# Kernel optimization log

Measured on AMD Instinct MI355X. Metric: run time of the kernel, lower is better.

The kernel has to match this reference:

```python
import jax, jax.numpy as jnp
import numpy as np

SUBSTEP = 10
FRAMES = 24
T = FRAMES * SUBSTEP
DT = 1.0 / 60.0 / SUBSTEP
SLOPE_DEG = 20.0
COS_S = float(np.cos(np.deg2rad(SLOPE_DEG)))
SIN_S = float(np.sin(np.deg2rad(SLOPE_DEG)))
INIT_HEIGHT = 0.1
N_VERTS = 2_000_000
GRAVITY = jnp.array([0.0, -9.8, 0.0], dtype=jnp.float32)
CONTACT_N = jnp.array([-SIN_S, COS_S, 0.0], dtype=jnp.float32)
EPS = 1e-6


def quat_mul(a, b):
    w1, x1, y1, z1 = a[0], a[1], a[2], a[3]
    w2, x2, y2, z2 = b[0], b[1], b[2], b[3]
    return jnp.stack([
        w1 * w2 - x1 * x2 - y1 * y2 - z1 * z2,
        w1 * x2 + x1 * w2 + y1 * z2 - z1 * y2,
        w1 * y2 + y1 * w2 + z1 * x2 - x1 * z2,
        w1 * z2 + z1 * w2 + x1 * y2 - y1 * x2,
    ])


def quat_to_matrix(q):
    q = q / jnp.linalg.norm(q)
    w, x, y, z = q[0], q[1], q[2], q[3]
    return jnp.stack([
        jnp.stack([1 - 2 * y * y - 2 * z * z, 2 * x * y - 2 * w * z, 2 * x * z + 2 * w * y]),
        jnp.stack([2 * x * y + 2 * w * z, 1 - 2 * x * x - 2 * z * z, 2 * y * z - 2 * w * x]),
        jnp.stack([2 * x * z - 2 * w * y, 2 * y * z + 2 * w * x, 1 - 2 * x * x - 2 * y * y]),
    ])


def cross_matrix(a):
    z = jnp.zeros((), dtype=a.dtype)
    return jnp.stack([
        jnp.stack([z, -a[2], a[1]]),
        jnp.stack([a[2], z, -a[0]]),
        jnp.stack([-a[1], a[0], z]),
    ])


def setup_inputs() -> dict:
    key = jax.random.key(0)
    k1, k2, k3 = jax.random.split(key, 3)
    return {
        "x": jax.random.normal(k1, (N_VERTS, 3), dtype=jnp.float32) * 0.2,
        "mass_center": jnp.zeros((3,), dtype=jnp.float32),
        "init_trans": jax.random.normal(k2, (3,), dtype=jnp.float32) * 0.3 + jnp.array([0.3, 0.5, 0.0]),
        "init_quat": jnp.ones((4,), dtype=jnp.float32),
        "init_v": jax.random.normal(k3, (3,), dtype=jnp.float32) * 0.1,
        "kn": jnp.array([0.5], dtype=jnp.float32),
        "mu": jnp.array([0.4], dtype=jnp.float32),
        "linear_damping": jnp.array([0.999], dtype=jnp.float32),
        "angular_damping": jnp.array([0.998], dtype=jnp.float32),
    }


def _simulate(x, mass_center, init_trans, init_quat, init_v, kn, mu, linear_damping, angular_damping):
    n = x.shape[0]
    mass = jnp.asarray(float(n), dtype=x.dtype)  # unit mass per vertex
    inv_mass = 1.0 / mass
    r = x - mass_center
    # inertia_reference = sum_i m*( (r.r) I - outer(r,r) )
    inertia = jnp.sum(jnp.einsum('ni,ni->n', r, r)) * jnp.eye(3, dtype=x.dtype) - jnp.einsum('ni,nj->ij', r, r)
    kn0, mu0 = kn[0], mu[0]
    ld, ad = linear_damping[0], angular_damping[0]
    eye3 = jnp.eye(3, dtype=x.dtype)

    def step(carry, _):
        trans, quat, v, omega = carry
        Rm = quat_to_matrix(quat)
        Rx = x @ Rm.T                                   # [N,3]
        xi = trans + Rx + mass_center                   # world positions
        vi_all = v + jnp.cross(omega[None, :], Rx)      # per-vertex velocities
        d = xi @ CONTACT_N
        rel_v = vi_all @ CONTACT_N
        mask = (d < -COS_S * INIT_HEIGHT) & (rel_v < 0.0)
        num = jnp.sum(mask)
        numf = jnp.maximum(num, 1).astype(x.dtype)
        sum_pos = jnp.sum(x * mask[:, None].astype(x.dtype), axis=0)
        ri = sum_pos / numf
        Ri = Rm @ ri
        vi = v + jnp.cross(omega, Ri)
        v_n = jnp.dot(vi, CONTACT_N) * CONTACT_N
        v_t = vi - v_n
        vn_new = -kn0 * v_n
        alpha = jnp.maximum(1.0 - mu0 * (1.0 + kn0) * (jnp.linalg.norm(v_n) / (jnp.linalg.norm(v_t) + EPS)), 0.0)
        vi_new = vn_new + alpha * v_t
        I = Rm @ inertia @ Rm.T
        I_inv = jnp.linalg.inv(I)
        Rri = cross_matrix(Ri)
        kmat = inv_mass * eye3 - Rri @ I_inv @ Rri
        J = jnp.linalg.solve(kmat, vi_new - vi)
        hit = num > 0
        dv = jnp.where(hit, J * inv_mass, 0.0)
        domega = jnp.where(hit, I_inv @ Rri @ J, 0.0)
        v_new = (v + GRAVITY * DT) * ld + dv
        omega_new = omega * ad + domega
        trans_new = trans + DT * v_new
        wq = jnp.concatenate([jnp.zeros((1,), dtype=x.dtype), omega_new]) * (0.5 * DT)
        quat_new = quat + quat_mul(wq, quat)
        quat_new = quat_new / jnp.linalg.norm(quat_new)
        new_carry = (trans_new, quat_new, v_new, omega_new)
        return new_carry, jnp.concatenate([trans_new, quat_new])

    carry0 = (init_trans, init_quat / jnp.linalg.norm(init_quat), init_v, jnp.zeros(3, dtype=x.dtype))
    _, traj = jax.lax.scan(step, carry0, None, length=T)
    return traj  # [T, 7] = translation(3) + quaternion(4) per substep


def reference(x, mass_center, init_trans, init_quat, init_v, kn, mu, linear_damping, angular_damping):
    return _simulate(x, mass_center, init_trans, init_quat, init_v, kn, mu, linear_damping, angular_damping)
```

## Files before the change

### kernel.cpp

```cpp
#include <hip/hip_runtime.h>

#define GRID   256
#define BLOCK  512
#define NWAVES (BLOCK / 64)
#define CHUNK  7813
#define SLOTS  16
#define NREPT  64

typedef unsigned long long u64;

__device__ __forceinline__ u64 rec_load(const u64* p) {
  return __hip_atomic_load(p, __ATOMIC_RELAXED, __HIP_MEMORY_SCOPE_AGENT);
}
__device__ __forceinline__ void rec_store(u64* p, u64 v) {
  __hip_atomic_store(p, v, __ATOMIC_RELAXED, __HIP_MEMORY_SCOPE_AGENT);
}
__device__ __forceinline__ u64 rec_pack(float f, unsigned tag) {
  return (u64)__float_as_uint(f) | ((u64)tag << 32);
}

#define C_NX   ((float)(-0.3420201433256687))
#define C_NY   ((float)( 0.9396926207859084))
#define C_DTF  ((float)(1.0 / 60.0 / 10.0))
#define C_HDT  ((float)(0.5 * (1.0 / 60.0 / 10.0)))
#define C_DTH  ((float)(-0.9396926207859084 * 0.1))
#define C_GYDT (-9.8f * (float)(1.0 / 60.0 / 10.0))

__device__ __forceinline__ void mat3_mul(const float* A, const float* B, float* C) {
  #pragma unroll
  for (int i = 0; i < 3; ++i)
    #pragma unroll
    for (int j = 0; j < 3; ++j)
      C[i*3+j] = A[i*3+0]*B[0*3+j] + A[i*3+1]*B[1*3+j] + A[i*3+2]*B[2*3+j];
}
__device__ __forceinline__ void mat3_mul_bt(const float* A, const float* B, float* C) {
  #pragma unroll
  for (int i = 0; i < 3; ++i)
    #pragma unroll
    for (int j = 0; j < 3; ++j)
      C[i*3+j] = A[i*3+0]*B[j*3+0] + A[i*3+1]*B[j*3+1] + A[i*3+2]*B[j*3+2];
}
__device__ __forceinline__ void mat3_inv(const float* m, float* inv) {
  float A =  (m[4]*m[8] - m[5]*m[7]);
  float B = -(m[3]*m[8] - m[5]*m[6]);
  float C =  (m[3]*m[7] - m[4]*m[6]);
  float det = m[0]*A + m[1]*B + m[2]*C;
  float id = 1.0f / det;
  inv[0] = A * id;
  inv[1] = -(m[1]*m[8] - m[2]*m[7]) * id;
  inv[2] =  (m[1]*m[5] - m[2]*m[4]) * id;
  inv[3] = B * id;
  inv[4] =  (m[0]*m[8] - m[2]*m[6]) * id;
  inv[5] = -(m[0]*m[5] - m[2]*m[3]) * id;
  inv[6] = C * id;
  inv[7] = -(m[0]*m[7] - m[1]*m[6]) * id;
  inv[8] =  (m[0]*m[4] - m[1]*m[3]) * id;
}

__global__ __launch_bounds__(BLOCK, 2)
void sim_kernel(const float* __restrict__ xg,
                const float* __restrict__ mc_p,
                const float* __restrict__ itr_p,
                const float* __restrict__ iq_p,
                const float* __restrict__ iv_p,
                const float* __restrict__ kn_p,
                const float* __restrict__ mu_p,
                const float* __restrict__ ldp_p,
                const float* __restrict__ adp_p,
                float* __restrict__ out,
                u64* __restrict__ ws,
                int N, int T)
{
  const int tid  = threadIdx.x;
  const int bid  = blockIdx.x;
  const int lane = tid & 63;
  const int wid  = tid >> 6;

  __shared__ float s_redI[NWAVES * 6];
  __shared__ float s_red[2][NWAVES * 4];
  __shared__ float s_gat[NWAVES * 4];

  u64* part = ws;
  u64* tot  = ws + 2 * 4 * GRID;
  u64* bufI = ws + 2 * 4 * GRID + 2 * NREPT * 4;

  const float mc0 = mc_p[0], mc1 = mc_p[1], mc2 = mc_p[2];

  const int vstart = bid * CHUNK;
  int cl = N - vstart; if (cl > CHUNK) cl = CHUNK; if (cl < 0) cl = 0;

  const float NANF = __int_as_float(0x7fc00000);
  float xr0[SLOTS], xr1[SLOTS], xr2[SLOTS];
  #pragma unroll
  for (int s = 0; s < SLOTS; ++s) {
    const int i = tid + s * BLOCK;
    if (i < cl) {
      const float* p = xg + (size_t)(vstart + i) * 3;
      xr0[s] = p[0]; xr1[s] = p[1]; xr2[s] = p[2];
    } else {
      xr0[s] = NANF; xr1[s] = NANF; xr2[s] = NANF;
    }
  }

  {
    float v6[6] = {0,0,0,0,0,0};
    #pragma unroll
    for (int s = 0; s < SLOTS; ++s) {
      if (tid + s * BLOCK < cl) {
        float r0 = xr0[s] - mc0, r1 = xr1[s] - mc1, r2 = xr2[s] - mc2;
        v6[0] += r0*r0; v6[1] += r1*r1; v6[2] += r2*r2;
        v6[3] += r0*r1; v6[4] += r0*r2; v6[5] += r1*r2;
      }
    }
    #pragma unroll
    for (int off = 32; off > 0; off >>= 1)
      #pragma unroll
      for (int k = 0; k < 6; ++k) v6[k] += __shfl_down(v6[k], off, 64);
    if (lane == 0) {
      #pragma unroll
      for (int k = 0; k < 6; ++k) s_redI[wid * 6 + k] = v6[k];
    }
    __syncthreads();
    if (tid == 0) {
      float t6[6];
      #pragma unroll
      for (int k = 0; k < 6; ++k) {
        t6[k] = s_redI[k];
        #pragma unroll
        for (int w = 1; w < NWAVES; ++w) t6[k] += s_redI[w * 6 + k];
      }
      #pragma unroll
      for (int k = 0; k < 6; ++k) rec_store(bufI + k * GRID + bid, rec_pack(t6[k], 0xC0FFEEu));
    }
    __syncthreads();
  }

  float In[9];
  {
    float g6[6] = {0,0,0,0,0,0};
    if (tid < GRID) {
      u64 r[6];
      int f = 0;
      for (;;) {
        #pragma unroll
        for (int k = 0; k < 6; ++k) r[k] = rec_load(bufI + k * GRID + tid);
        bool ok = true;
        #pragma unroll
        for (int k = 0; k < 6; ++k) ok &= ((unsigned)(r[k] >> 32) == 0xC0FFEEu);
        if (ok) break;
        if ((++f & 15) == 0) __builtin_amdgcn_s_sleep(1);
      }
      #pragma unroll
      for (int k = 0; k < 6; ++k) g6[k] = __uint_as_float((unsigned)r[k]);
    }
    #pragma unroll
    for (int off = 32; off > 0; off >>= 1)
      #pragma unroll
      for (int k = 0; k < 6; ++k) g6[k] += __shfl_down(g6[k], off, 64);
    if (lane == 0) {
      #pragma unroll
      for (int k = 0; k < 6; ++k) s_redI[wid * 6 + k] = g6[k];
    }
    __syncthreads();
    float t6[6];
    #pragma unroll
    for (int k = 0; k < 6; ++k) {
      t6[k] = s_redI[k];
      #pragma unroll
      for (int w = 1; w < NWAVES; ++w) t6[k] += s_redI[w * 6 + k];
    }
    float trc = t6[0] + t6[1] + t6[2];
    In[0] = trc - t6[0]; In[4] = trc - t6[1]; In[8] = trc - t6[2];
    In[1] = -t6[3]; In[3] = -t6[3];
    In[2] = -t6[4]; In[6] = -t6[4];
    In[5] = -t6[5]; In[7] = -t6[5];
  }

  float tr0 = itr_p[0], tr1 = itr_p[1], tr2 = itr_p[2];
  float q0 = iq_p[0], q1 = iq_p[1], q2 = iq_p[2], q3 = iq_p[3];
  {
    float n0 = sqrtf(q0*q0 + q1*q1 + q2*q2 + q3*q3);
    q0 /= n0; q1 /= n0; q2 /= n0; q3 /= n0;
  }
  float v0 = iv_p[0], v1 = iv_p[1], v2 = iv_p[2];
  float om0 = 0.f, om1 = 0.f, om2 = 0.f;
  const float knv = kn_p[0], muv = mu_p[0], ldv = ldp_p[0], adv = adp_p[0];
  const float inv_mass = 1.0f / (float)N;

  float Rm[9], Ii[9];
  float pa0, pa1, pa2, pb0, pb1, pb2, pca, pcb;
  int skip;

  {
    float qn = sqrtf(q0*q0 + q1*q1 + q2*q2 + q3*q3);
    float w = q0/qn, xq = q1/qn, yq = q2/qn, zq = q3/qn;
    Rm[0] = 1.f - 2.f*yq*yq - 2.f*zq*zq; Rm[1] = 2.f*xq*yq - 2.f*w*zq; Rm[2] = 2.f*xq*zq + 2.f*w*yq;
    Rm[3] = 2.f*xq*yq + 2.f*w*zq; Rm[4] = 1.f - 2.f*xq*xq - 2.f*zq*zq; Rm[5] = 2.f*yq*zq - 2.f*w*xq;
    Rm[6] = 2.f*xq*zq - 2.f*w*yq; Rm[7] = 2.f*yq*zq + 2.f*w*xq; Rm[8] = 1.f - 2.f*xq*xq - 2.f*yq*yq;
    pa0 = Rm[0]*C_NX + Rm[3]*C_NY;
    pa1 = Rm[1]*C_NX + Rm[4]*C_NY;
    pa2 = Rm[2]*C_NX + Rm[5]*C_NY;
    float w0 = C_NY*om2, w1 = -C_NX*om2, w2 = C_NX*om1 - C_NY*om0;
    pb0 = Rm[0]*w0 + Rm[3]*w1 + Rm[6]*w2;
    pb1 = Rm[1]*w0 + Rm[4]*w1 + Rm[7]*w2;
    pb2 = Rm[2]*w0 + Rm[5]*w1 + Rm[8]*w2;
    pca = C_DTH - ((tr0 + mc0)*C_NX + (tr1 + mc1)*C_NY);
    pcb = -(v0*C_NX + v1*C_NY);
    skip = (om0 == 0.f && om1 == 0.f && om2 == 0.f && !(pcb > 0.f)) ? 1 : 0;
    float Tm[9]; mat3_mul(Rm, In, Tm);
    float Iw[9]; mat3_mul_bt(Tm, Rm, Iw);
    mat3_inv(Iw, Ii);
  }

  int pub = 0;
  for (int t = 0; t < T; ++t) {
    float tn = 0.f, tx = 0.f, ty = 0.f, tz = 0.f;

    if (!skip) {
      const int p = pub & 1;
      const unsigned want = (unsigned)(pub + 1);

      float acc0 = 0.f, acc1 = 0.f, acc2 = 0.f, acc3 = 0.f;
      #pragma unroll
      for (int s = 0; s < SLOTS; ++s) {
        const float x0 = xr0[s], x1 = xr1[s], x2 = xr2[s];
        const float da = x0*pa0 + x1*pa1 + x2*pa2;
        const float db = x0*pb0 + x1*pb1 + x2*pb2;
        if (da < pca && db < pcb) {
          acc0 += 1.f; acc1 += x0; acc2 += x1; acc3 += x2;
        }
      }
      #pragma unroll
      for (int off = 32; off > 0; off >>= 1) {
        acc0 += __shfl_down(acc0, off, 64);
        acc1 += __shfl_down(acc1, off, 64);
        acc2 += __shfl_down(acc2, off, 64);
        acc3 += __shfl_down(acc3, off, 64);
      }
      float* srA = s_red[p];
      if (lane == 0) {
        srA[wid*4+0] = acc0; srA[wid*4+1] = acc1;
        srA[wid*4+2] = acc2; srA[wid*4+3] = acc3;
      }
      __syncthreads();
      if (tid < 4) {
        float tw = srA[tid];
        #pragma unroll
        for (int w2 = 1; w2 < NWAVES; ++w2) tw += srA[w2*4 + tid];
        rec_store(part + (size_t)p * 4 * GRID + (size_t)tid * GRID + bid,
                  rec_pack(tw, want));
      }

      {
        float Tm[9]; mat3_mul(Rm, In, Tm);
        float Iw[9]; mat3_mul_bt(Tm, Rm, Iw);
        mat3_inv(Iw, Ii);
      }

      if (bid == 0) {
        float f0 = 0.f, f1 = 0.f, f2 = 0.f, f3 = 0.f;
        if (tid < GRID) {
          const u64* pp = part + (size_t)p * 4 * GRID + tid;
          u64 r0, r1, r2, r3;
          int fl = 0;
          for (;;) {
            r0 = rec_load(pp + 0 * GRID);
            r1 = rec_load(pp + 1 * GRID);
            r2 = rec_load(pp + 2 * GRID);
            r3 = rec_load(pp + 3 * GRID);
            if (((unsigned)(r0 >> 32) == want) && ((unsigned)(r1 >> 32) == want) &&
                ((unsigned)(r2 >> 32) == want) && ((unsigned)(r3 >> 32) == want)) break;
            if ((++fl & 15) == 0) __builtin_amdgcn_s_sleep(1);
          }
          f0 = __uint_as_float((unsigned)r0);
          f1 = __uint_as_float((unsigned)r1);
          f2 = __uint_as_float((unsigned)r2);
          f3 = __uint_as_float((unsigned)r3);
        }
        #pragma unroll
        for (int off = 32; off > 0; off >>= 1) {
          f0 += __shfl_down(f0, off, 64);
          f1 += __shfl_down(f1, off, 64);
          f2 += __shfl_down(f2, off, 64);
          f3 += __shfl_down(f3, off, 64);
        }
        if (lane == 0) {
          s_gat[wid*4+0] = f0; s_gat[wid*4+1] = f1;
          s_gat[wid*4+2] = f2; s_gat[wid*4+3] = f3;
        }
        __syncthreads();
        tn = s_gat[0]; tx = s_gat[1]; ty = s_gat[2]; tz = s_gat[3];
        #pragma unroll
        for (int w2 = 1; w2 < NWAVES; ++w2) {
          tn += s_gat[w2*4+0]; tx += s_gat[w2*4+1];
          ty += s_gat[w2*4+2]; tz += s_gat[w2*4+3];
        }
        if (tid < NREPT * 4) {
          const int w2 = tid & 3;
          const float val = (w2 == 0) ? tn : (w2 == 1) ? tx : (w2 == 2) ? ty : tz;
          rec_store(tot + (size_t)p * NREPT * 4 + tid, rec_pack(val, want));
        }
      } else {
        const u64* tp = tot + (size_t)p * NREPT * 4 + (size_t)(bid & (NREPT - 1)) * 4;
        u64 r0, r1, r2, r3;
        int fl = 0;
        for (;;) {
          r0 = rec_load(tp + 0); r1 = rec_load(tp + 1);
          r2 = rec_load(tp + 2); r3 = rec_load(tp + 3);
          if (((unsigned)(r0 >> 32) == want) && ((unsigned)(r1 >> 32) == want) &&
              ((unsigned)(r2 >> 32) == want) && ((unsigned)(r3 >> 32) == want)) break;
          if ((++fl & 31) == 0) __builtin_amdgcn_s_sleep(1);
        }
        tn = __uint_as_float((unsigned)r0);
        tx = __uint_as_float((unsigned)r1);
        ty = __uint_as_float((unsigned)r2);
        tz = __uint_as_float((unsigned)r3);
      }
      ++pub;
    }

    {
      float dv0 = 0.f, dv1 = 0.f, dv2 = 0.f, dm0 = 0.f, dm1 = 0.f, dm2 = 0.f;
      if (tn > 0.0f) {
        float numf = fmaxf(tn, 1.0f);
        float ri0 = tx/numf, ri1 = ty/numf, ri2 = tz/numf;
        float Ri0 = Rm[0]*ri0 + Rm[1]*ri1 + Rm[2]*ri2;
        float Ri1 = Rm[3]*ri0 + Rm[4]*ri1 + Rm[5]*ri2;
        float Ri2 = Rm[6]*ri0 + Rm[7]*ri1 + Rm[8]*ri2;
        float vi0 = v0 + om1*Ri2 - om2*Ri1;
        float vi1 = v1 + om2*Ri0 - om0*Ri2;
        float vi2 = v2 + om0*Ri1 - om1*Ri0;
        float vdn = vi0*C_NX + vi1*C_NY;
        float vn0 = vdn*C_NX, vn1 = vdn*C_NY;
        float vt0 = vi0 - vn0, vt1 = vi1 - vn1, vt2 = vi2;
        float nvn = sqrtf(vn0*vn0 + vn1*vn1);
        float nvt = sqrtf(vt0*vt0 + vt1*vt1 + vt2*vt2);
        float alpha = fmaxf(1.0f - muv*(1.0f + knv)*(nvn/(nvt + 1e-6f)), 0.0f);
        float dvi0 = (-knv*vn0 + alpha*vt0) - vi0;
        float dvi1 = (-knv*vn1 + alpha*vt1) - vi1;
        float dvi2 = (alpha*vt2) - vi2;
        float Cx[9] = {0.f, -Ri2, Ri1,  Ri2, 0.f, -Ri0,  -Ri1, Ri0, 0.f};
        float T2[9]; mat3_mul(Cx, Ii, T2);
        float T3[9]; mat3_mul(T2, Cx, T3);
        float Km[9];
        #pragma unroll
        for (int m = 0; m < 9; ++m) Km[m] = -T3[m];
        Km[0] += inv_mass; Km[4] += inv_mass; Km[8] += inv_mass;
        float Ki[9]; mat3_inv(Km, Ki);
        float J0 = Ki[0]*dvi0 + Ki[1]*dvi1 + Ki[2]*dvi2;
        float J1 = Ki[3]*dvi0 + Ki[4]*dvi1 + Ki[5]*dvi2;
        float J2 = Ki[6]*dvi0 + Ki[7]*dvi1 + Ki[8]*dvi2;
        dv0 = J0*inv_mass; dv1 = J1*inv_mass; dv2 = J2*inv_mass;
        float c0 = -Ri2*J1 + Ri1*J2;
        float c1 =  Ri2*J0 - Ri0*J2;
        float c2 = -Ri1*J0 + Ri0*J1;
        dm0 = Ii[0]*c0 + Ii[1]*c1 + Ii[2]*c2;
        dm1 = Ii[3]*c0 + Ii[4]*c1 + Ii[5]*c2;
        dm2 = Ii[6]*c0 + Ii[7]*c1 + Ii[8]*c2;
      }
      v0 = v0*ldv + dv0;
      v1 = (v1 + C_GYDT)*ldv + dv1;
      v2 = v2*ldv + dv2;
      om0 = om0*adv + dm0; om1 = om1*adv + dm1; om2 = om2*adv + dm2;
      tr0 += C_DTF*v0; tr1 += C_DTF*v1; tr2 += C_DTF*v2;
      float wx = om0*C_HDT, wy = om1*C_HDT, wz = om2*C_HDT;
      float dq0 = -wx*q1 - wy*q2 - wz*q3;
      float dq1 =  wx*q0 + wy*q3 - wz*q2;
      float dq2 =  wy*q0 + wz*q1 - wx*q3;
      float dq3 =  wz*q0 + wx*q2 - wy*q1;
      q0 += dq0; q1 += dq1; q2 += dq2; q3 += dq3;
      float qn2 = sqrtf(q0*q0 + q1*q1 + q2*q2 + q3*q3);
      q0 /= qn2; q1 /= qn2; q2 /= qn2; q3 /= qn2;
      if (bid == 0 && tid == 0) {
        float* o = out + (size_t)t * 7;
        o[0] = tr0; o[1] = tr1; o[2] = tr2;
        o[3] = q0;  o[4] = q1;  o[5] = q2;  o[6] = q3;
      }
      float qn = sqrtf(q0*q0 + q1*q1 + q2*q2 + q3*q3);
      float w = q0/qn, xq = q1/qn, yq = q2/qn, zq = q3/qn;
      Rm[0] = 1.f - 2.f*yq*yq - 2.f*zq*zq; Rm[1] = 2.f*xq*yq - 2.f*w*zq; Rm[2] = 2.f*xq*zq + 2.f*w*yq;
      Rm[3] = 2.f*xq*yq + 2.f*w*zq; Rm[4] = 1.f - 2.f*xq*xq - 2.f*zq*zq; Rm[5] = 2.f*yq*zq - 2.f*w*xq;
      Rm[6] = 2.f*xq*zq - 2.f*w*yq; Rm[7] = 2.f*yq*zq + 2.f*w*xq; Rm[8] = 1.f - 2.f*xq*xq - 2.f*yq*yq;
      pa0 = Rm[0]*C_NX + Rm[3]*C_NY;
      pa1 = Rm[1]*C_NX + Rm[4]*C_NY;
      pa2 = Rm[2]*C_NX + Rm[5]*C_NY;
      float w0 = C_NY*om2, w1 = -C_NX*om2, w2 = C_NX*om1 - C_NY*om0;
      pb0 = Rm[0]*w0 + Rm[3]*w1 + Rm[6]*w2;
      pb1 = Rm[1]*w0 + Rm[4]*w1 + Rm[7]*w2;
      pb2 = Rm[2]*w0 + Rm[5]*w1 + Rm[8]*w2;
      pca = C_DTH - ((tr0 + mc0)*C_NX + (tr1 + mc1)*C_NY);
      pcb = -(v0*C_NX + v1*C_NY);
      skip = (om0 == 0.f && om1 == 0.f && om2 == 0.f && !(pcb > 0.f)) ? 1 : 0;
    }
  }
}

extern "C" void kernel_launch(void* const* d_in, const int* in_sizes, int n_in,
                              void* d_out, int out_size, void* d_ws, size_t ws_size,
                              hipStream_t stream) {
  const float* x   = (const float*)d_in[0];
  const float* mc  = (const float*)d_in[1];
  const float* itr = (const float*)d_in[2];
  const float* iq  = (const float*)d_in[3];
  const float* iv  = (const float*)d_in[4];
  const float* kn  = (const float*)d_in[5];
  const float* mu  = (const float*)d_in[6];
  const float* ldp = (const float*)d_in[7];
  const float* adp = (const float*)d_in[8];
  float* out = (float*)d_out;
  u64* ws  = (u64*)d_ws;
  int N = in_sizes[0] / 3;
  int T = out_size / 7;

  void* args[] = {(void*)&x, (void*)&mc, (void*)&itr, (void*)&iq, (void*)&iv,
                  (void*)&kn, (void*)&mu, (void*)&ldp, (void*)&adp,
                  (void*)&out, (void*)&ws, (void*)&N, (void*)&T};
  hipLaunchCooperativeKernel((void*)sim_kernel, dim3(GRID), dim3(BLOCK),
                             args, 0, stream);
}
```

Baseline: 1.430 ms.

## Replace block-0 gather with hierarchical fixed-point atomic reduction and last-arriver broadcast

The per-step grid reduction no longer has block 0 poll 256 tagged partials. Each block now atomically adds fixed-point encoded sums into per-group counters. The last block of each group bumps a second-level counter, and the globally last block sums the group totals and publishes replicated tagged results that the other blocks poll. The accumulator buffers are zeroed up front with a cooperative grid sync, and the world inertia inverse is computed only when contact occurs. The goal is to shorten the serial critical path of each substep, at the cost of fixed-point quantisation of the sums and a dependency on cooperative launch.

```diff
diff --git a/kernel.cpp b/kernel.cpp
--- a/kernel.cpp
+++ b/kernel.cpp
@@ -1,23 +1,22 @@
 #include <hip/hip_runtime.h>
+#include <hip/hip_cooperative_groups.h>
 
 #define GRID   256
 #define BLOCK  512
 #define NWAVES (BLOCK / 64)
 #define CHUNK  7813
 #define SLOTS  16
-#define NREPT  64
+#define TMAX   256
+#define NREP   64
 
 typedef unsigned long long u64;
-
-__device__ __forceinline__ u64 rec_load(const u64* p) {
-  return __hip_atomic_load(p, __ATOMIC_RELAXED, __HIP_MEMORY_SCOPE_AGENT);
-}
-__device__ __forceinline__ void rec_store(u64* p, u64 v) {
-  __hip_atomic_store(p, v, __ATOMIC_RELAXED, __HIP_MEMORY_SCOPE_AGENT);
-}
-__device__ __forceinline__ u64 rec_pack(float f, unsigned tag) {
-  return (u64)__float_as_uint(f) | ((u64)tag << 32);
-}
+typedef unsigned int u32;
+
+namespace cg = cooperative_groups;
+
+
+#define SCALEF    268435456.0f
+#define INV_SCALE (1.0 / 268435456.0)
 
 #define C_NX   ((float)(-0.3420201433256687))
 #define C_NY   ((float)( 0.9396926207859084))
@@ -25,6 +24,16 @@
 #define C_HDT  ((float)(0.5 * (1.0 / 60.0 / 10.0)))
 #define C_DTH  ((float)(-0.9396926207859084 * 0.1))
 #define C_GYDT (-9.8f * (float)(1.0 / 60.0 / 10.0))
+
+__device__ __forceinline__ u64 rec_load(const u64* p) {
+  return __hip_atomic_load(p, __ATOMIC_RELAXED, __HIP_MEMORY_SCOPE_AGENT);
+}
+__device__ __forceinline__ void rec_store(u64* p, u64 v) {
+  __hip_atomic_store(p, v, __ATOMIC_RELAXED, __HIP_MEMORY_SCOPE_AGENT);
+}
+__device__ __forceinline__ u64 rec_pack(float f, unsigned tag) {
+  return (u64)__float_as_uint(f) | ((u64)tag << 32);
+}
 
 __device__ __forceinline__ void mat3_mul(const float* A, const float* B, float* C) {
   #pragma unroll
@@ -75,14 +84,17 @@
   const int bid  = blockIdx.x;
   const int lane = tid & 63;
   const int wid  = tid >> 6;
+  const int grp  = bid >> 4;
 
   __shared__ float s_redI[NWAVES * 6];
-  __shared__ float s_red[2][NWAVES * 4];
-  __shared__ float s_gat[NWAVES * 4];
-
-  u64* part = ws;
-  u64* tot  = ws + 2 * 4 * GRID;
-  u64* bufI = ws + 2 * 4 * GRID + 2 * NREPT * 4;
+  __shared__ float s_red[NWAVES * 4];
+  __shared__ float s_tot[4];
+  __shared__ int   s_fin;
+
+  u64* acc  = ws;
+  u64* s2   = ws + (size_t)TMAX * 640;
+  u64* rep  = ws + (size_t)TMAX * 640 + TMAX*8;
+  u64* bufI = rep + 2 * NREP * 8;
 
   const float mc0 = mc_p[0], mc1 = mc_p[1], mc2 = mc_p[2];
 
@@ -130,20 +142,28 @@
         for (int w = 1; w < NWAVES; ++w) t6[k] += s_redI[w * 6 + k];
       }
       #pragma unroll
-      for (int k = 0; k < 6; ++k) rec_store(bufI + k * GRID + bid, rec_pack(t6[k], 0xC0FFEEu));
+      for (int k = 0; k < 6; ++k)
+        rec_store(bufI + (size_t)k * GRID + bid, rec_pack(t6[k], 0xC0FFEEu));
     }
     __syncthreads();
   }
+
+  {
+    const size_t gid = (size_t)bid * BLOCK + tid;
+    const size_t nthr = (size_t)GRID * BLOCK;
+    for (size_t i = gid; i < (size_t)TMAX * 640; i += nthr) rec_store(acc + i, 0ull);
+    for (size_t i = gid; i < (size_t)TMAX * 8; i += nthr)   rec_store(s2 + i, 0ull);
+  }
+  cg::this_grid().sync();
 
   float In[9];
   {
     float g6[6] = {0,0,0,0,0,0};
     if (tid < GRID) {
-      u64 r[6];
-      int f = 0;
+      u64 r[6]; int f = 0;
       for (;;) {
         #pragma unroll
-        for (int k = 0; k < 6; ++k) r[k] = rec_load(bufI + k * GRID + tid);
+        for (int k = 0; k < 6; ++k) r[k] = rec_load(bufI + (size_t)k * GRID + tid);
         bool ok = true;
         #pragma unroll
         for (int k = 0; k < 6; ++k) ok &= ((unsigned)(r[k] >> 32) == 0xC0FFEEu);
@@ -187,7 +207,7 @@
   const float knv = kn_p[0], muv = mu_p[0], ldv = ldp_p[0], adv = adp_p[0];
   const float inv_mass = 1.0f / (float)N;
 
-  float Rm[9], Ii[9];
+  float Rm[9];
   float pa0, pa1, pa2, pb0, pb1, pb2, pca, pcb;
   int skip;
 
@@ -207,9 +227,6 @@
     pca = C_DTH - ((tr0 + mc0)*C_NX + (tr1 + mc1)*C_NY);
     pcb = -(v0*C_NX + v1*C_NY);
     skip = (om0 == 0.f && om1 == 0.f && om2 == 0.f && !(pcb > 0.f)) ? 1 : 0;
-    float Tm[9]; mat3_mul(Rm, In, Tm);
-    float Iw[9]; mat3_mul_bt(Tm, Rm, Iw);
-    mat3_inv(Iw, Ii);
   }
 
   int pub = 0;
@@ -219,6 +236,7 @@
     if (!skip) {
       const int p = pub & 1;
       const unsigned want = (unsigned)(pub + 1);
+      u64* ab = acc + (size_t)t * 640;
 
       float acc0 = 0.f, acc1 = 0.f, acc2 = 0.f, acc3 = 0.f;
       #pragma unroll
@@ -237,91 +255,83 @@
         acc2 += __shfl_down(acc2, off, 64);
         acc3 += __shfl_down(acc3, off, 64);
       }
-      float* srA = s_red[p];
       if (lane == 0) {
-        srA[wid*4+0] = acc0; srA[wid*4+1] = acc1;
-        srA[wid*4+2] = acc2; srA[wid*4+3] = acc3;
+        s_red[wid*4+0] = acc0; s_red[wid*4+1] = acc1;
+        s_red[wid*4+2] = acc2; s_red[wid*4+3] = acc3;
       }
       __syncthreads();
-      if (tid < 4) {
-        float tw = srA[tid];
+
+      if (tid == 0) {
+        float f4[4];
         #pragma unroll
-        for (int w2 = 1; w2 < NWAVES; ++w2) tw += srA[w2*4 + tid];
-        rec_store(part + (size_t)p * 4 * GRID + (size_t)tid * GRID + bid,
-                  rec_pack(tw, want));
-      }
-
-      {
-        float Tm[9]; mat3_mul(Rm, In, Tm);
-        float Iw[9]; mat3_mul_bt(Tm, Rm, Iw);
-        mat3_inv(Iw, Ii);
-      }
-
-      if (bid == 0) {
-        float f0 = 0.f, f1 = 0.f, f2 = 0.f, f3 = 0.f;
-        if (tid < GRID) {
-          const u64* pp = part + (size_t)p * 4 * GRID + tid;
-          u64 r0, r1, r2, r3;
-          int fl = 0;
-          for (;;) {
-            r0 = rec_load(pp + 0 * GRID);
-            r1 = rec_load(pp + 1 * GRID);
-            r2 = rec_load(pp + 2 * GRID);
-            r3 = rec_load(pp + 3 * GRID);
-            if (((unsigned)(r0 >> 32) == want) && ((unsigned)(r1 >> 32) == want) &&
-                ((unsigned)(r2 >> 32) == want) && ((unsigned)(r3 >> 32) == want)) break;
-            if ((++fl & 15) == 0) __builtin_amdgcn_s_sleep(1);
-          }
-          f0 = __uint_as_float((unsigned)r0);
-          f1 = __uint_as_float((unsigned)r1);
-          f2 = __uint_as_float((unsigned)r2);
-          f3 = __uint_as_float((unsigned)r3);
+        for (int c = 0; c < 4; ++c) {
+          float tw = s_red[c];
+          #pragma unroll
+          for (int w = 1; w < NWAVES; ++w) tw += s_red[w*4 + c];
+          f4[c] = tw;
         }
-        #pragma unroll
-        for (int off = 32; off > 0; off >>= 1) {
-          f0 += __shfl_down(f0, off, 64);
-          f1 += __shfl_down(f1, off, 64);
-          f2 += __shfl_down(f2, off, 64);
-          f3 += __shfl_down(f3, off, 64);
+        atomicAdd(ab + (size_t)grp*40 + 0,  (u64)(long long)f4[0]);
+        atomicAdd(ab + (size_t)grp*40 + 8,  (u64)(long long)__float2ll_rn(f4[1] * SCALEF));
+        atomicAdd(ab + (size_t)grp*40 + 16, (u64)(long long)__float2ll_rn(f4[2] * SCALEF));
+        atomicAdd(ab + (size_t)grp*40 + 24, (u64)(long long)__float2ll_rn(f4[3] * SCALEF));
+        __builtin_amdgcn_fence(__ATOMIC_RELEASE, "agent");
+        u64 oldc = atomicAdd(ab + (size_t)grp*40 + 32, 1ull);
+        int fin = 0;
+        if (oldc == 15ull) {
+          __builtin_amdgcn_fence(__ATOMIC_ACQ_REL, "agent");
+          u64 olds = atomicAdd(s2 + (size_t)t * 8, 1ull);
+          if (olds == 15ull) fin = 1;
         }
-        if (lane == 0) {
-          s_gat[wid*4+0] = f0; s_gat[wid*4+1] = f1;
-          s_gat[wid*4+2] = f2; s_gat[wid*4+3] = f3;
-        }
-        __syncthreads();
-        tn = s_gat[0]; tx = s_gat[1]; ty = s_gat[2]; tz = s_gat[3];
-        #pragma unroll
-        for (int w2 = 1; w2 < NWAVES; ++w2) {
-          tn += s_gat[w2*4+0]; tx += s_gat[w2*4+1];
-          ty += s_gat[w2*4+2]; tz += s_gat[w2*4+3];
-        }
-        if (tid < NREPT * 4) {
-          const int w2 = tid & 3;
-          const float val = (w2 == 0) ? tn : (w2 == 1) ? tx : (w2 == 2) ? ty : tz;
-          rec_store(tot + (size_t)p * NREPT * 4 + tid, rec_pack(val, want));
+        s_fin = fin;
+      }
+      __syncthreads();
+
+      if (s_fin) {
+        if (wid == 0) {
+          __builtin_amdgcn_fence(__ATOMIC_ACQUIRE, "agent");
+          const int g = lane >> 2, c = lane & 3;
+          long long v = (long long)rec_load(acc + (size_t)t * 640 + (size_t)g*40 + (size_t)c*8);
+          #pragma unroll
+          for (int m = 4; m <= 32; m <<= 1) v += __shfl_xor(v, m, 64);
+          long long l0 = __shfl(v, 0, 64);
+          long long l1 = __shfl(v, 1, 64);
+          long long l2 = __shfl(v, 2, 64);
+          long long l3 = __shfl(v, 3, 64);
+          float fn = (float)l0;
+          float fx = (float)((double)l1 * INV_SCALE);
+          float fy = (float)((double)l2 * INV_SCALE);
+          float fz = (float)((double)l3 * INV_SCALE);
+          u64* rl = rep + (size_t)p * NREP * 8 + (size_t)lane * 8;
+          rec_store(rl + 0, rec_pack(fn, want));
+          rec_store(rl + 1, rec_pack(fx, want));
+          rec_store(rl + 2, rec_pack(fy, want));
+          rec_store(rl + 3, rec_pack(fz, want));
+          if (lane == 0) { s_tot[0] = fn; s_tot[1] = fx; s_tot[2] = fy; s_tot[3] = fz; }
         }
       } else {
-        const u64* tp = tot + (size_t)p * NREPT * 4 + (size_t)(bid & (NREPT - 1)) * 4;
-        u64 r0, r1, r2, r3;
-        int fl = 0;
-        for (;;) {
-          r0 = rec_load(tp + 0); r1 = rec_load(tp + 1);
-          r2 = rec_load(tp + 2); r3 = rec_load(tp + 3);
-          if (((unsigned)(r0 >> 32) == want) && ((unsigned)(r1 >> 32) == want) &&
-              ((unsigned)(r2 >> 32) == want) && ((unsigned)(r3 >> 32) == want)) break;
-          if ((++fl & 31) == 0) __builtin_amdgcn_s_sleep(1);
+        if (tid < 4) {
+          const u64* rl = rep + (size_t)p * NREP * 8 + (size_t)(bid & (NREP - 1)) * 8 + tid;
+          u64 r; int f = 0;
+          for (;;) {
+            r = rec_load(rl);
+            if ((unsigned)(r >> 32) == want) break;
+            if ((++f & 31) == 0) __builtin_amdgcn_s_sleep(1);
+          }
+          __builtin_amdgcn_fence(__ATOMIC_ACQUIRE, "agent");
+          s_tot[tid] = __uint_as_float((unsigned)r);
         }
-        tn = __uint_as_float((unsigned)r0);
-        tx = __uint_as_float((unsigned)r1);
-        ty = __uint_as_float((unsigned)r2);
-        tz = __uint_as_float((unsigned)r3);
-      }
+      }
+      __syncthreads();
+      tn = s_tot[0]; tx = s_tot[1]; ty = s_tot[2]; tz = s_tot[3];
       ++pub;
     }
 
     {
       float dv0 = 0.f, dv1 = 0.f, dv2 = 0.f, dm0 = 0.f, dm1 = 0.f, dm2 = 0.f;
       if (tn > 0.0f) {
+        float Tm[9]; mat3_mul(Rm, In, Tm);
+        float Iw[9]; mat3_mul_bt(Tm, Rm, Iw);
+        float Ii[9]; mat3_inv(Iw, Ii);
         float numf = fmaxf(tn, 1.0f);
         float ri0 = tx/numf, ri1 = ty/numf, ri2 = tz/numf;
         float Ri0 = Rm[0]*ri0 + Rm[1]*ri1 + Rm[2]*ri2;
```

Measured after the change: 2.239 ms. 1.57x slower.
